# Kernel optimization log

Hardware: AMD Instinct MI355X
Metric: run time of the kernel (lower is better)

## Reference

```python
import jax, jax.numpy as jnp
import numpy as np

B, T, E, S, W, H = 2, 2048, 256, 128, 8, 150

def _mlp(x, w1, b1, w2, b2, w3, b3):
    # Score module: Linear->ReLU->Linear->ReLU->Linear (dropout inactive in eval)
    h = jax.nn.relu(x @ w1 + b1)
    h = jax.nn.relu(h @ w2 + b2)
    return h @ w3 + b3

def _mlp_params(key, d_in):
    k1, k2, k3 = jax.random.split(key, 3)
    s = 0.02
    return (s * jax.random.normal(k1, (d_in, H), jnp.float32), jnp.zeros((H,), jnp.float32),
            s * jax.random.normal(k2, (H, H), jnp.float32), jnp.zeros((H,), jnp.float32),
            s * jax.random.normal(k3, (H, 1), jnp.float32), jnp.zeros((1,), jnp.float32))

def setup_inputs() -> dict:
    key = jax.random.key(0)
    ke, ks, ka, km, kp = jax.random.split(key, 5)
    inp = {
        'batch_embeds': jax.random.normal(ke, (B, T, E), jnp.float32),
        'span_starts': jax.random.randint(ks, (B, S), 0, T - W, jnp.int32),
    }
    for name, k, d in [('attn', ka, E), ('ment', km, 3 * E), ('pair', kp, 9 * E)]:
        w1, b1, w2, b2, w3, b3 = _mlp_params(k, d)
        inp.update({f'{name}_w1': w1, f'{name}_b1': b1, f'{name}_w2': w2,
                    f'{name}_b2': b2, f'{name}_w3': w3, f'{name}_b3': b3})
    return inp

def reference(batch_embeds, span_starts,
              attn_w1, attn_b1, attn_w2, attn_b2, attn_w3, attn_b3,
              ment_w1, ment_b1, ment_w2, ment_b2, ment_w3, ment_b3,
              pair_w1, pair_b1, pair_w2, pair_b2, pair_w3, pair_b3):
    # ---- MentionScore ----
    attns = _mlp(batch_embeds, attn_w1, attn_b1, attn_w2, attn_b2, attn_w3, attn_b3)  # [B,T,1]
    spans = span_starts[:, :, None] + jnp.arange(W)                                   # [B,S,W]
    flat = spans.reshape(B, S * W)
    emb_spans = jnp.take_along_axis(batch_embeds, flat[:, :, None], axis=1).reshape(B, S, W, E)
    attn_spans = jnp.take_along_axis(attns, flat[:, :, None], axis=1).reshape(B, S, W, 1)
    start = emb_spans[:, :, 0, :]
    end = emb_spans[:, :, -1, :]
    weighted = jnp.sum(emb_spans * attn_spans, axis=2)                                # [B,S,E]
    g_i = jnp.concatenate([start, end, weighted], axis=-1)                            # [B,S,3E]
    mention_scores = _mlp(g_i, ment_w1, ment_b1, ment_w2, ment_b2, ment_w3, ment_b3)  # [B,S,1]
    # ---- PairwiseScore: all-pairs cat(g_i, g_j, g_i*g_j) ----
    gi = jnp.broadcast_to(g_i[:, :, None, :], (B, S, S, 3 * E))
    gj = jnp.broadcast_to(g_i[:, None, :, :], (B, S, S, 3 * E))
    pairs = jnp.concatenate([gi, gj, gi * gj], axis=-1)                               # [B,S,S,9E]
    pair_scores = _mlp(pairs, pair_w1, pair_b1, pair_w2, pair_b2, pair_w3, pair_b3)   # [B,S,S,1]
    # extended score = mean(mention_i, mention_j, pair_ij)
    ext = (mention_scores[:, :, None, :] + mention_scores[:, None, :, :] + pair_scores) / 3.0
    return ext
```

## Files before the change

kernel.cpp:

```cpp
#include <hip/hip_runtime.h>
#include <hip/hip_bf16.h>


typedef __bf16 bf16;
typedef __attribute__((ext_vector_type(8))) short v8s;
typedef __attribute__((ext_vector_type(8))) __bf16 v8bf;
typedef __attribute__((ext_vector_type(4))) float v4f;

#define MFMA_BF16(A, B, C) __builtin_amdgcn_mfma_f32_16x16x32_bf16((A), (B), (C), 0, 0, 0)

__device__ __forceinline__ v8bf mul_cvt8(float4 xa, float4 xb, float4 sa, float4 sb) {
    v8bf w;
    w[0] = (bf16)(xa.x * sa.x); w[1] = (bf16)(xa.y * sa.y);
    w[2] = (bf16)(xa.z * sa.z); w[3] = (bf16)(xa.w * sa.w);
    w[4] = (bf16)(xb.x * sb.x); w[5] = (bf16)(xb.y * sb.y);
    w[6] = (bf16)(xb.z * sb.z); w[7] = (bf16)(xb.w * sb.w);
    return w;
}
__device__ __forceinline__ v8bf cvt8(float4 xa, float4 xb) {
    v8bf w;
    w[0] = (bf16)xa.x; w[1] = (bf16)xa.y; w[2] = (bf16)xa.z; w[3] = (bf16)xa.w;
    w[4] = (bf16)xb.x; w[5] = (bf16)xb.y; w[6] = (bf16)xb.z; w[7] = (bf16)xb.w;
    return w;
}

__global__ __launch_bounds__(256) void prep_kernel(
    const float* __restrict__ pw1, const float* __restrict__ pw2,
    const float* __restrict__ aw1, const float* __restrict__ aw2,
    const float* __restrict__ mw1, const float* __restrict__ mw2,
    const float* __restrict__ pb1, const float* __restrict__ pb2, const float* __restrict__ pw3,
    const float* __restrict__ ab1, const float* __restrict__ ab2, const float* __restrict__ aw3,
    const float* __restrict__ mb1, const float* __restrict__ mb2, const float* __restrict__ mw3,
    bf16* __restrict__ w1cT, bf16* __restrict__ w2pT,
    bf16* __restrict__ w1aT, bf16* __restrict__ w2aT, bf16* __restrict__ w2mT,
    bf16* __restrict__ wuvmT, float* __restrict__ bias)
{
    int idx = blockIdx.x * 256 + threadIdx.x;
    if (idx < 147456) {
        int h = idx / 768, e = idx % 768;
        w1cT[idx] = (bf16)((h < 150) ? pw1[(1536 + e) * 150 + h] : 0.f);
    } else if (idx < 178176) {
        int j = idx - 147456; int n = j / 160, k = j % 160;
        w2pT[j] = (bf16)((n < 150 && k < 150) ? pw2[k * 150 + n] : 0.f);
    } else if (idx < 227328) {
        int j = idx - 178176; int h = j / 256, e = j % 256;
        w1aT[j] = (bf16)((h < 150) ? aw1[e * 150 + h] : 0.f);
    } else if (idx < 258048) {
        int j = idx - 227328; int n = j / 160, k = j % 160;
        w2aT[j] = (bf16)((n < 150 && k < 150) ? aw2[k * 150 + n] : 0.f);
    } else if (idx < 288768) {
        int j = idx - 258048; int n = j / 160, k = j % 160;
        w2mT[j] = (bf16)((n < 150 && k < 150) ? mw2[k * 150 + n] : 0.f);
    } else if (idx < 731136) {
        int j = idx - 288768; int s = j / 147456; int r = j % 147456;
        int h = r / 768, e = r % 768;
        float v = 0.f;
        if (h < 150) {
            if (s == 0)      v = pw1[e * 150 + h];
            else if (s == 1) v = pw1[(768 + e) * 150 + h];
            else             v = mw1[e * 150 + h];
        }
        wuvmT[j] = (bf16)v;
    } else if (idx < 732864) {
        int j = idx - 731136; int arr = j / 192, h = j % 192;
        const float* src;
        switch (arr) {
            case 0: src = pb1; break; case 1: src = pb2; break; case 2: src = pw3; break;
            case 3: src = ab1; break; case 4: src = ab2; break; case 5: src = aw3; break;
            case 6: src = mb1; break; case 7: src = mb2; break; default: src = mw3; break;
        }
        bias[j] = (h < 150) ? src[h] : 0.f;
    }
}

__global__ __launch_bounds__(256) void build_g_kernel(
    const float* __restrict__ emb, const int* __restrict__ spans,
    const float* __restrict__ attns, float* __restrict__ g)
{
    int blk = blockIdx.x;
    int b = blk >> 7;
    int t0 = spans[blk];
    int e = threadIdx.x;
    const float* eb = emb + ((size_t)(b * 2048 + t0)) * 256 + e;
    const float* at = attns + b * 2048 + t0;
    float start = eb[0];
    float endv  = eb[7 * 256];
    float wsum = 0.f;
#pragma unroll
    for (int w = 0; w < 8; ++w) wsum = fmaf(eb[w * 256], at[w], wsum);
    g[(size_t)blk * 768 + e]       = start;
    g[(size_t)blk * 768 + 256 + e] = endv;
    g[(size_t)blk * 768 + 512 + e] = wsum;
}

#define A32_ELEMS 2304
#define A64_ELEMS 4608
#define B_ELEMS   13824

__global__ __launch_bounds__(512, 4) void attn_mfma_kernel(
    const float* __restrict__ emb,
    const bf16* __restrict__ w1aT, const bf16* __restrict__ w2aT,
    const float* __restrict__ b1p, const float* __restrict__ b2p,
    const float* __restrict__ w3p, const float* __restrict__ b3,
    float* __restrict__ attns)
{
    __shared__ __attribute__((aligned(16))) char smem[64512];
    bf16*  a_lds  = (bf16*)smem;
    bf16*  b_lds  = (bf16*)(smem + 9216);
    bf16*  h1_lds = (bf16*)smem;
    float* red    = (float*)(smem + 10752);

    const int m0  = blockIdx.x * 32;
    const int tid = threadIdx.x;
    const int lane = tid & 63;
    const int wm = (tid >> 6) >> 2, wn = (tid >> 6) & 3;
    const int l15 = lane & 15, lk = (lane >> 4) * 8;
    const int aj = tid >> 3, ae = (tid & 7) * 8;
    const int br = tid >> 3, bc = (tid & 7) * 8;
    const float* gA = emb + (size_t)(m0 + (aj & 31)) * 256 + ae;

    v4f acc[3];
#pragma unroll
    for (int nf = 0; nf < 3; ++nf) acc[nf] = (v4f){0.f, 0.f, 0.f, 0.f};

#define ATTN_COMPUTE(AB, BB)                                                   \
    do {                                                                       \
        _Pragma("unroll")                                                      \
        for (int ks = 0; ks < 2; ++ks) {                                       \
            const int kb = ks * 32 + lk;                                       \
            v8s af = *(const v8s*)&(AB)[(wm * 16 + l15) * 72 + kb];            \
            v8s bf0 = *(const v8s*)&(BB)[(wn * 48 +  0 + l15) * 72 + kb];      \
            v8s bf1 = *(const v8s*)&(BB)[(wn * 48 + 16 + l15) * 72 + kb];      \
            v8s bf2 = *(const v8s*)&(BB)[(wn * 48 + 32 + l15) * 72 + kb];      \
            acc[0] = MFMA_BF16(af, bf0, acc[0]);                               \
            acc[1] = MFMA_BF16(af, bf1, acc[1]);                               \
            acc[2] = MFMA_BF16(af, bf2, acc[2]);                               \
        }                                                                      \
    } while (0)

    {
        if (tid < 256) {
            float4 x0 = *(const float4*)(gA + 0), x1 = *(const float4*)(gA + 4);
            *(v8bf*)(a_lds + aj * 72 + ae) = cvt8(x0, x1);
        }
#pragma unroll
        for (int s2 = 0; s2 < 3; ++s2) {
            const int row = br + s2 * 64;
            *(uint4*)(b_lds + row * 72 + bc) = *(const uint4*)(w1aT + row * 256 + bc);
        }
    }
    float4 xB0, xB1; uint4 bB0, bB1, bB2;
    if (tid < 256) { xB0 = *(const float4*)(gA + 64); xB1 = *(const float4*)(gA + 68); }
    bB0 = *(const uint4*)(w1aT + (br +   0) * 256 + 64 + bc);
    bB1 = *(const uint4*)(w1aT + (br +  64) * 256 + 64 + bc);
    bB2 = *(const uint4*)(w1aT + (br + 128) * 256 + 64 + bc);
    __syncthreads();

    float4 xA0, xA1; uint4 bA0, bA1, bA2;
    for (int cc = 0; cc < 2; ++cc) {
        const int c = cc * 2;
        if (cc < 1) {
            const int e0 = (c + 2) * 64;
            if (tid < 256) { xA0 = *(const float4*)(gA + e0); xA1 = *(const float4*)(gA + e0 + 4); }
            bA0 = *(const uint4*)(w1aT + (br +   0) * 256 + e0 + bc);
            bA1 = *(const uint4*)(w1aT + (br +  64) * 256 + e0 + bc);
            bA2 = *(const uint4*)(w1aT + (br + 128) * 256 + e0 + bc);
        }
        ATTN_COMPUTE(a_lds, b_lds);
        if (tid < 256)
            *(v8bf*)(a_lds + A32_ELEMS + aj * 72 + ae) = cvt8(xB0, xB1);
        *(uint4*)(b_lds + B_ELEMS + (br +   0) * 72 + bc) = bB0;
        *(uint4*)(b_lds + B_ELEMS + (br +  64) * 72 + bc) = bB1;
        *(uint4*)(b_lds + B_ELEMS + (br + 128) * 72 + bc) = bB2;
        __syncthreads();
        if (cc < 1) {
            const int e0 = (c + 3) * 64;
            if (tid < 256) { xB0 = *(const float4*)(gA + e0); xB1 = *(const float4*)(gA + e0 + 4); }
            bB0 = *(const uint4*)(w1aT + (br +   0) * 256 + e0 + bc);
            bB1 = *(const uint4*)(w1aT + (br +  64) * 256 + e0 + bc);
            bB2 = *(const uint4*)(w1aT + (br + 128) * 256 + e0 + bc);
        }
        ATTN_COMPUTE(a_lds + A32_ELEMS, b_lds + B_ELEMS);
        if (cc < 1) {
            if (tid < 256)
                *(v8bf*)(a_lds + aj * 72 + ae) = cvt8(xA0, xA1);
            *(uint4*)(b_lds + (br +   0) * 72 + bc) = bA0;
            *(uint4*)(b_lds + (br +  64) * 72 + bc) = bA1;
            *(uint4*)(b_lds + (br + 128) * 72 + bc) = bA2;
        }
        __syncthreads();
    }

    {
        const float b10 = b1p[wn * 48 + 0  + l15];
        const float b11 = b1p[wn * 48 + 16 + l15];
        const float b12 = b1p[wn * 48 + 32 + l15];
#pragma unroll
        for (int r = 0; r < 4; ++r) {
            const int jl = wm * 16 + (lane >> 4) * 4 + r;
            bf16* hrow = h1_lds + jl * 168 + wn * 48 + l15;
            hrow[0] = (bf16)fmaxf(acc[0][r] + b10, 0.f);
            if (wn < 3) {
                hrow[16] = (bf16)fmaxf(acc[1][r] + b11, 0.f);
                hrow[32] = (bf16)fmaxf(acc[2][r] + b12, 0.f);
            }
        }
    }
    __syncthreads();

    v4f acc2[3];
#pragma unroll
    for (int nf = 0; nf < 3; ++nf) acc2[nf] = (v4f){0.f, 0.f, 0.f, 0.f};
#pragma unroll
    for (int ks = 0; ks < 5; ++ks) {
        const int kb = ks * 32 + lk;
        v8s af = *(const v8s*)&h1_lds[(wm * 16 + l15) * 168 + kb];
        v8s bfr[3];
#pragma unroll
        for (int nf = 0; nf < 3; ++nf)
            bfr[nf] = *(const v8s*)&w2aT[(size_t)(wn * 48 + nf * 16 + l15) * 160 + kb];
#pragma unroll
        for (int nf = 0; nf < 3; ++nf)
            acc2[nf] = MFMA_BF16(af, bfr[nf], acc2[nf]);
    }

    const float b2v0 = b2p[wn * 48 + 0  + l15], w3v0 = w3p[wn * 48 + 0  + l15];
    const float b2v1 = b2p[wn * 48 + 16 + l15], w3v1 = w3p[wn * 48 + 16 + l15];
    const float b2v2 = b2p[wn * 48 + 32 + l15], w3v2 = w3p[wn * 48 + 32 + l15];
#pragma unroll
    for (int r = 0; r < 4; ++r) {
        float p = fmaxf(acc2[0][r] + b2v0, 0.f) * w3v0
                + fmaxf(acc2[1][r] + b2v1, 0.f) * w3v1
                + fmaxf(acc2[2][r] + b2v2, 0.f) * w3v2;
        p += __shfl_xor(p, 1);
        p += __shfl_xor(p, 2);
        p += __shfl_xor(p, 4);
        p += __shfl_xor(p, 8);
        if (l15 == 0) {
            const int jl = wm * 16 + (lane >> 4) * 4 + r;
            red[jl * 4 + wn] = p;
        }
    }
    __syncthreads();
    if (tid < 32) {
        attns[m0 + tid] = red[tid * 4 + 0] + red[tid * 4 + 1]
                        + red[tid * 4 + 2] + red[tid * 4 + 3] + b3[0];
    }
}

__global__ __launch_bounds__(512, 4) void uvm_mfma_kernel(
    const float* __restrict__ g, const bf16* __restrict__ wuvmT,
    const bf16* __restrict__ w2mT,
    const float* __restrict__ pb1p, const float* __restrict__ mb1p,
    const float* __restrict__ mb2p, const float* __restrict__ mw3p,
    const float* __restrict__ mb3,
    float* __restrict__ u_pad, float* __restrict__ v_pad, float* __restrict__ ment)
{
    __shared__ __attribute__((aligned(16))) char smem[64512];
    bf16*  a_lds  = (bf16*)smem;
    bf16*  b_lds  = (bf16*)(smem + 9216);
    bf16*  h1_lds = (bf16*)smem;
    float* red    = (float*)(smem + 10752);

    const int sect = blockIdx.x >> 3;
    const int m0   = (blockIdx.x & 7) * 32;
    const bf16* Bw = wuvmT + (size_t)sect * 147456;
    const int tid = threadIdx.x;
    const int lane = tid & 63;
    const int wm = (tid >> 6) >> 2, wn = (tid >> 6) & 3;
    const int l15 = lane & 15, lk = (lane >> 4) * 8;
    const int aj = tid >> 3, ae = (tid & 7) * 8;
    const int br = tid >> 3, bc = (tid & 7) * 8;
    const float* gA = g + (size_t)(m0 + (aj & 31)) * 768 + ae;

    v4f acc[3];
#pragma unroll
    for (int nf = 0; nf < 3; ++nf) acc[nf] = (v4f){0.f, 0.f, 0.f, 0.f};

    {
        if (tid < 256) {
            float4 x0 = *(const float4*)(gA + 0), x1 = *(const float4*)(gA + 4);
            *(v8bf*)(a_lds + aj * 72 + ae) = cvt8(x0, x1);
        }
#pragma unroll
        for (int s2 = 0; s2 < 3; ++s2) {
            const int row = br + s2 * 64;
            *(uint4*)(b_lds + row * 72 + bc) = *(const uint4*)(Bw + row * 768 + bc);
        }
    }
    float4 xB0, xB1; uint4 bB0, bB1, bB2;
    if (tid < 256) { xB0 = *(const float4*)(gA + 64); xB1 = *(const float4*)(gA + 68); }
    bB0 = *(const uint4*)(Bw + (br +   0) * 768 + 64 + bc);
    bB1 = *(const uint4*)(Bw + (br +  64) * 768 + 64 + bc);
    bB2 = *(const uint4*)(Bw + (br + 128) * 768 + 64 + bc);
    __syncthreads();

    float4 xA0, xA1; uint4 bA0, bA1, bA2;
    for (int cc = 0; cc < 6; ++cc) {
        const int c = cc * 2;
        if (cc < 5) {
            const int e0 = (c + 2) * 64;
            if (tid < 256) { xA0 = *(const float4*)(gA + e0); xA1 = *(const float4*)(gA + e0 + 4); }
            bA0 = *(const uint4*)(Bw + (br +   0) * 768 + e0 + bc);
            bA1 = *(const uint4*)(Bw + (br +  64) * 768 + e0 + bc);
            bA2 = *(const uint4*)(Bw + (br + 128) * 768 + e0 + bc);
        }
        ATTN_COMPUTE(a_lds, b_lds);
        if (tid < 256)
            *(v8bf*)(a_lds + A32_ELEMS + aj * 72 + ae) = cvt8(xB0, xB1);
        *(uint4*)(b_lds + B_ELEMS + (br +   0) * 72 + bc) = bB0;
        *(uint4*)(b_lds + B_ELEMS + (br +  64) * 72 + bc) = bB1;
        *(uint4*)(b_lds + B_ELEMS + (br + 128) * 72 + bc) = bB2;
        __syncthreads();
        if (cc < 5) {
            const int e0 = (c + 3) * 64;
            if (tid < 256) { xB0 = *(const float4*)(gA + e0); xB1 = *(const float4*)(gA + e0 + 4); }
            bB0 = *(const uint4*)(Bw + (br +   0) * 768 + e0 + bc);
            bB1 = *(const uint4*)(Bw + (br +  64) * 768 + e0 + bc);
            bB2 = *(const uint4*)(Bw + (br + 128) * 768 + e0 + bc);
        }
        ATTN_COMPUTE(a_lds + A32_ELEMS, b_lds + B_ELEMS);
        if (cc < 5) {
            if (tid < 256)
                *(v8bf*)(a_lds + aj * 72 + ae) = cvt8(xA0, xA1);
            *(uint4*)(b_lds + (br +   0) * 72 + bc) = bA0;
            *(uint4*)(b_lds + (br +  64) * 72 + bc) = bA1;
            *(uint4*)(b_lds + (br + 128) * 72 + bc) = bA2;
        }
        __syncthreads();
    }

    if (sect < 2) {
        float* dst = (sect == 0) ? u_pad : v_pad;
        const float bb0 = (sect == 0) ? pb1p[wn * 48 + 0  + l15] : 0.f;
        const float bb1 = (sect == 0) ? pb1p[wn * 48 + 16 + l15] : 0.f;
        const float bb2 = (sect == 0) ? pb1p[wn * 48 + 32 + l15] : 0.f;
#pragma unroll
        for (int r = 0; r < 4; ++r) {
            const int jl = wm * 16 + (lane >> 4) * 4 + r;
            float* drow = dst + (size_t)(m0 + jl) * 192 + wn * 48 + l15;
            drow[0]  = acc[0][r] + bb0;
            drow[16] = acc[1][r] + bb1;
            drow[32] = acc[2][r] + bb2;
        }
        return;
    }

    {
        const float b10 = mb1p[wn * 48 + 0  + l15];
        const float b11 = mb1p[wn * 48 + 16 + l15];
        const float b12 = mb1p[wn * 48 + 32 + l15];
#pragma unroll
        for (int r = 0; r < 4; ++r) {
            const int jl = wm * 16 + (lane >> 4) * 4 + r;
            bf16* hrow = h1_lds + jl * 168 + wn * 48 + l15;
            hrow[0] = (bf16)fmaxf(acc[0][r] + b10, 0.f);
            if (wn < 3) {
                hrow[16] = (bf16)fmaxf(acc[1][r] + b11, 0.f);
                hrow[32] = (bf16)fmaxf(acc[2][r] + b12, 0.f);
            }
        }
    }
    __syncthreads();

    v4f acc2[3];
#pragma unroll
    for (int nf = 0; nf < 3; ++nf) acc2[nf] = (v4f){0.f, 0.f, 0.f, 0.f};
#pragma unroll
    for (int ks = 0; ks < 5; ++ks) {
        const int kb = ks * 32 + lk;
        v8s af = *(const v8s*)&h1_lds[(wm * 16 + l15) * 168 + kb];
        v8s bfr[3];
#pragma unroll
        for (int nf = 0; nf < 3; ++nf)
            bfr[nf] = *(const v8s*)&w2mT[(size_t)(wn * 48 + nf * 16 + l15) * 160 + kb];
#pragma unroll
        for (int nf = 0; nf < 3; ++nf)
            acc2[nf] = MFMA_BF16(af, bfr[nf], acc2[nf]);
    }

    const float b2v0 = mb2p[wn * 48 + 0  + l15], w3v0 = mw3p[wn * 48 + 0  + l15];
    const float b2v1 = mb2p[wn * 48 + 16 + l15], w3v1 = mw3p[wn * 48 + 16 + l15];
    const float b2v2 = mb2p[wn * 48 + 32 + l15], w3v2 = mw3p[wn * 48 + 32 + l15];
#pragma unroll
    for (int r = 0; r < 4; ++r) {
        float p = fmaxf(acc2[0][r] + b2v0, 0.f) * w3v0
                + fmaxf(acc2[1][r] + b2v1, 0.f) * w3v1
                + fmaxf(acc2[2][r] + b2v2, 0.f) * w3v2;
        p += __shfl_xor(p, 1);
        p += __shfl_xor(p, 2);
        p += __shfl_xor(p, 4);
        p += __shfl_xor(p, 8);
        if (l15 == 0) {
            const int jl = wm * 16 + (lane >> 4) * 4 + r;
            red[jl * 4 + wn] = p;
        }
    }
    __syncthreads();
    if (tid < 32) {
        ment[m0 + tid] = red[tid * 4 + 0] + red[tid * 4 + 1]
                       + red[tid * 4 + 2] + red[tid * 4 + 3] + mb3[0];
    }
}

__global__ __launch_bounds__(512, 4) void pair_mfma_kernel(
    const float* __restrict__ g,
    const float* __restrict__ u_pad, const float* __restrict__ v_pad,
    const bf16* __restrict__ w1cT, const bf16* __restrict__ w2T,
    const float* __restrict__ b2_pad, const float* __restrict__ w3_pad,
    const float* __restrict__ pb3, const float* __restrict__ ment,
    float* __restrict__ out)
{
    __shared__ __attribute__((aligned(16))) char smem[76800];
    bf16*  a_lds  = (bf16*)smem;
    bf16*  b_lds  = (bf16*)(smem + 18432);
    float* gi_s   = (float*)(smem + 73728);
    bf16*  h1_lds = (bf16*)smem;
    float* red    = (float*)(smem + 22528);

    const int blk = blockIdx.x;
    const int b = blk >> 8;
    const int i = (blk >> 1) & 127;
    const int half = blk & 1;
    const int row_i = b * 128 + i;
    const int jg0 = b * 128 + half * 64;
    const int tid = threadIdx.x;
    const int lane = tid & 63;
    const int wm = (tid >> 6) >> 2, wn = (tid >> 6) & 3;
    const int l15 = lane & 15, lk = (lane >> 4) * 8;
    const int aj = tid >> 3, ae = (tid & 7) * 8;
    const int br = tid >> 3, bc = (tid & 7) * 8;
    const float* gA = g + (size_t)(jg0 + aj) * 768 + ae;

    if (tid < 192)
        *(float4*)&gi_s[tid * 4] = *(const float4*)&g[(size_t)row_i * 768 + tid * 4];
    __syncthreads();

    v4f acc[2][3];
#pragma unroll
    for (int mf = 0; mf < 2; ++mf)
#pragma unroll
        for (int nf = 0; nf < 3; ++nf) acc[mf][nf] = (v4f){0.f, 0.f, 0.f, 0.f};

#define PAIR_COMPUTE(AB, BB)                                                   \
    do {                                                                       \
        _Pragma("unroll")                                                      \
        for (int ks = 0; ks < 2; ++ks) {                                       \
            const int kb = ks * 32 + lk;                                       \
            v8s af0 = *(const v8s*)&(AB)[(wm * 32 +  0 + l15) * 72 + kb];      \
            v8s af1 = *(const v8s*)&(AB)[(wm * 32 + 16 + l15) * 72 + kb];      \
            v8s bf0 = *(const v8s*)&(BB)[(wn * 48 +  0 + l15) * 72 + kb];      \
            v8s bf1 = *(const v8s*)&(BB)[(wn * 48 + 16 + l15) * 72 + kb];      \
            v8s bf2 = *(const v8s*)&(BB)[(wn * 48 + 32 + l15) * 72 + kb];      \
            acc[0][0] = MFMA_BF16(af0, bf0, acc[0][0]);                        \
            acc[0][1] = MFMA_BF16(af0, bf1, acc[0][1]);                        \
            acc[0][2] = MFMA_BF16(af0, bf2, acc[0][2]);                        \
            acc[1][0] = MFMA_BF16(af1, bf0, acc[1][0]);                        \
            acc[1][1] = MFMA_BF16(af1, bf1, acc[1][1]);                        \
            acc[1][2] = MFMA_BF16(af1, bf2, acc[1][2]);                        \
        }                                                                      \
    } while (0)

    {
        float4 x0 = *(const float4*)(gA + 0), x1 = *(const float4*)(gA + 4);
        const float* gp = gi_s + ae;
        float4 s0 = *(const float4*)(gp + 0), s1 = *(const float4*)(gp + 4);
        *(v8bf*)(a_lds + aj * 72 + ae) = mul_cvt8(x0, x1, s0, s1);
#pragma unroll
        for (int s2 = 0; s2 < 3; ++s2) {
            const int row = br + s2 * 64;
            *(uint4*)(b_lds + row * 72 + bc) = *(const uint4*)(w1cT + row * 768 + bc);
        }
    }
    float4 xB0, xB1; uint4 bB0, bB1, bB2;
    xB0 = *(const float4*)(gA + 64);
    xB1 = *(const float4*)(gA + 68);
    bB0 = *(const uint4*)(w1cT + (br +   0) * 768 + 64 + bc);
    bB1 = *(const uint4*)(w1cT + (br +  64) * 768 + 64 + bc);
    bB2 = *(const uint4*)(w1cT + (br + 128) * 768 + 64 + bc);
    __syncthreads();

    float4 xA0, xA1; uint4 bA0, bA1, bA2;
    for (int cc = 0; cc < 6; ++cc) {
        const int c = cc * 2;
        if (cc < 5) {
            const int e0 = (c + 2) * 64;
            xA0 = *(const float4*)(gA + e0);
            xA1 = *(const float4*)(gA + e0 + 4);
            bA0 = *(const uint4*)(w1cT + (br +   0) * 768 + e0 + bc);
            bA1 = *(const uint4*)(w1cT + (br +  64) * 768 + e0 + bc);
            bA2 = *(const uint4*)(w1cT + (br + 128) * 768 + e0 + bc);
        }
        PAIR_COMPUTE(a_lds, b_lds);
        {
            const float* gp = gi_s + (c + 1) * 64 + ae;
            float4 s0 = *(const float4*)(gp + 0), s1 = *(const float4*)(gp + 4);
            *(v8bf*)(a_lds + A64_ELEMS + aj * 72 + ae) = mul_cvt8(xB0, xB1, s0, s1);
            *(uint4*)(b_lds + B_ELEMS + (br +   0) * 72 + bc) = bB0;
            *(uint4*)(b_lds + B_ELEMS + (br +  64) * 72 + bc) = bB1;
            *(uint4*)(b_lds + B_ELEMS + (br + 128) * 72 + bc) = bB2;
        }
        __syncthreads();
        if (cc < 5) {
            const int e0 = (c + 3) * 64;
            xB0 = *(const float4*)(gA + e0);
            xB1 = *(const float4*)(gA + e0 + 4);
            bB0 = *(const uint4*)(w1cT + (br +   0) * 768 + e0 + bc);
            bB1 = *(const uint4*)(w1cT + (br +  64) * 768 + e0 + bc);
            bB2 = *(const uint4*)(w1cT + (br + 128) * 768 + e0 + bc);
        }
        PAIR_COMPUTE(a_lds + A64_ELEMS, b_lds + B_ELEMS);
        if (cc < 5) {
            const float* gp = gi_s + (c + 2) * 64 + ae;
            float4 s0 = *(const float4*)(gp + 0), s1 = *(const float4*)(gp + 4);
            *(v8bf*)(a_lds + aj * 72 + ae) = mul_cvt8(xA0, xA1, s0, s1);
            *(uint4*)(b_lds + (br +   0) * 72 + bc) = bA0;
            *(uint4*)(b_lds + (br +  64) * 72 + bc) = bA1;
            *(uint4*)(b_lds + (br + 128) * 72 + bc) = bA2;
        }
        __syncthreads();
    }

    {
        const float uh0 = u_pad[row_i * 192 + wn * 48 + 0  + l15];
        const float uh1 = u_pad[row_i * 192 + wn * 48 + 16 + l15];
        const float uh2 = u_pad[row_i * 192 + wn * 48 + 32 + l15];
#pragma unroll
        for (int mf = 0; mf < 2; ++mf) {
#pragma unroll
            for (int r = 0; r < 4; ++r) {
                const int jl = wm * 32 + mf * 16 + (lane >> 4) * 4 + r;
                const float* vrow = v_pad + (size_t)(jg0 + jl) * 192 + wn * 48 + l15;
                const float v0 = acc[mf][0][r] + uh0 + vrow[0];
                const float v1 = acc[mf][1][r] + uh1 + vrow[16];
                const float v2 = acc[mf][2][r] + uh2 + vrow[32];
                bf16* hrow = h1_lds + jl * 168 + wn * 48 + l15;
                hrow[0] = (bf16)fmaxf(v0, 0.f);
                if (wn < 3) {
                    hrow[16] = (bf16)fmaxf(v1, 0.f);
                    hrow[32] = (bf16)fmaxf(v2, 0.f);
                }
            }
        }
    }
    __syncthreads();

    v4f acc2[2][3];
#pragma unroll
    for (int mf = 0; mf < 2; ++mf)
#pragma unroll
        for (int nf = 0; nf < 3; ++nf) acc2[mf][nf] = (v4f){0.f, 0.f, 0.f, 0.f};
#pragma unroll
    for (int ks = 0; ks < 5; ++ks) {
        const int kb = ks * 32 + lk;
        v8s af[2], bfr[3];
#pragma unroll
        for (int mf = 0; mf < 2; ++mf)
            af[mf] = *(const v8s*)&h1_lds[(wm * 32 + mf * 16 + l15) * 168 + kb];
#pragma unroll
        for (int nf = 0; nf < 3; ++nf)
            bfr[nf] = *(const v8s*)&w2T[(size_t)(wn * 48 + nf * 16 + l15) * 160 + kb];
#pragma unroll
        for (int mf = 0; mf < 2; ++mf)
#pragma unroll
            for (int nf = 0; nf < 3; ++nf)
                acc2[mf][nf] = MFMA_BF16(af[mf], bfr[nf], acc2[mf][nf]);
    }

    const float b2v0 = b2_pad[wn * 48 + 0  + l15], w3v0 = w3_pad[wn * 48 + 0  + l15];
    const float b2v1 = b2_pad[wn * 48 + 16 + l15], w3v1 = w3_pad[wn * 48 + 16 + l15];
    const float b2v2 = b2_pad[wn * 48 + 32 + l15], w3v2 = w3_pad[wn * 48 + 32 + l15];
#pragma unroll
    for (int mf = 0; mf < 2; ++mf) {
#pragma unroll
        for (int r = 0; r < 4; ++r) {
            float p = fmaxf(acc2[mf][0][r] + b2v0, 0.f) * w3v0
                    + fmaxf(acc2[mf][1][r] + b2v1, 0.f) * w3v1
                    + fmaxf(acc2[mf][2][r] + b2v2, 0.f) * w3v2;
            p += __shfl_xor(p, 1);
            p += __shfl_xor(p, 2);
            p += __shfl_xor(p, 4);
            p += __shfl_xor(p, 8);
            if (l15 == 0) {
                const int jl = wm * 32 + mf * 16 + (lane >> 4) * 4 + r;
                red[jl * 4 + wn] = p;
            }
        }
    }
    __syncthreads();
    if (tid < 64) {
        const float s = red[tid * 4 + 0] + red[tid * 4 + 1] + red[tid * 4 + 2] + red[tid * 4 + 3];
        out[(size_t)b * 16384 + (size_t)i * 128 + half * 64 + tid] =
            (s + pb3[0] + ment[row_i] + ment[b * 128 + half * 64 + tid]) * (1.f / 3.f);
    }
}

extern "C" void kernel_launch(void* const* d_in, const int* in_sizes, int n_in,
                              void* d_out, int out_size, void* d_ws, size_t ws_size,
                              hipStream_t stream)
{
    const float* emb   = (const float*)d_in[0];
    const int*   spans = (const int*)d_in[1];
    const float* aw1 = (const float*)d_in[2];
    const float* ab1 = (const float*)d_in[3];
    const float* aw2 = (const float*)d_in[4];
    const float* ab2 = (const float*)d_in[5];
    const float* aw3 = (const float*)d_in[6];
    const float* ab3 = (const float*)d_in[7];
    const float* mw1 = (const float*)d_in[8];
    const float* mb1 = (const float*)d_in[9];
    const float* mw2 = (const float*)d_in[10];
    const float* mb2 = (const float*)d_in[11];
    const float* mw3 = (const float*)d_in[12];
    const float* mb3 = (const float*)d_in[13];
    const float* pw1 = (const float*)d_in[14];
    const float* pb1 = (const float*)d_in[15];
    const float* pw2 = (const float*)d_in[16];
    const float* pb2 = (const float*)d_in[17];
    const float* pw3 = (const float*)d_in[18];
    const float* pb3 = (const float*)d_in[19];

    float* ws    = (float*)d_ws;
    float* attns = ws;
    float* g     = ws + 4096;
    float* ment  = ws + 200704;
    float* u_pad = ws + 200960;
    float* v_pad = ws + 250112;
    float* bias  = ws + 299264;
    float* pb1p = bias;         float* pb2p = bias + 192;  float* pw3p = bias + 384;
    float* ab1p = bias + 576;   float* ab2p = bias + 768;  float* aw3p = bias + 960;
    float* mb1p = bias + 1152;  float* mb2p = bias + 1344; float* mw3p = bias + 1536;
    bf16* w1cT  = (bf16*)(ws + 300992);
    bf16* w2pT  = (bf16*)(ws + 374720);
    bf16* w1aT  = (bf16*)(ws + 390080);
    bf16* w2aT  = (bf16*)(ws + 414656);
    bf16* w2mT  = (bf16*)(ws + 430016);
    bf16* wuvmT = (bf16*)(ws + 445376);

    prep_kernel<<<2863, 256, 0, stream>>>(pw1, pw2, aw1, aw2, mw1, mw2,
                                          pb1, pb2, pw3, ab1, ab2, aw3, mb1, mb2, mw3,
                                          w1cT, w2pT, w1aT, w2aT, w2mT, wuvmT, bias);
    attn_mfma_kernel<<<128, 512, 0, stream>>>(emb, w1aT, w2aT, ab1p, ab2p, aw3p, ab3, attns);
    build_g_kernel<<<256, 256, 0, stream>>>(emb, spans, attns, g);
    uvm_mfma_kernel<<<24, 512, 0, stream>>>(g, wuvmT, w2mT, pb1p, mb1p, mb2p, mw3p, mb3,
                                            u_pad, v_pad, ment);
    pair_mfma_kernel<<<512, 512, 0, stream>>>(g, u_pad, v_pad, w1cT, w2pT,
                                              pb2p, pw3p, pb3, ment, (float*)d_out);
}
```

Measured before the change: 57.67 us.

## Widen pair tile to 128 rows and load W1 fragments straight to registers

The pair kernel now handles all 128 j-rows for one i per block, which halves the grid to 256 blocks and doubles the M tile per wave (4 MFMA row fragments). The W1 fragments are no longer staged in LDS. Each wave loads its B operands directly from global memory into registers and prefetches the next chunk. This removes the LDS traffic for the weight tile, halves redundant weight loads across blocks, and shrinks shared memory. The trade-off is higher register pressure (launch bounds drop to 2 blocks per SM) and fewer blocks, which gives less parallelism on a GPU with many CUs.

```diff
diff --git a/kernel.cpp b/kernel.cpp
--- a/kernel.cpp
+++ b/kernel.cpp
@@ -94,7 +94,6 @@
 }
 
 #define A32_ELEMS 2304
-#define A64_ELEMS 4608
 #define B_ELEMS   13824
 
 __global__ __launch_bounds__(512, 4) void attn_mfma_kernel(
@@ -403,7 +402,8 @@
     }
 }
 
-__global__ __launch_bounds__(512, 4) void pair_mfma_kernel(
+#define A128_ELEMS 9216
+__global__ __launch_bounds__(512, 2) void pair_mfma_kernel(
     const float* __restrict__ g,
     const float* __restrict__ u_pad, const float* __restrict__ v_pad,
     const bf16* __restrict__ w1cT, const bf16* __restrict__ w2T,
@@ -411,112 +411,92 @@
     const float* __restrict__ pb3, const float* __restrict__ ment,
     float* __restrict__ out)
 {
-    __shared__ __attribute__((aligned(16))) char smem[76800];
+    __shared__ __attribute__((aligned(16))) char smem[45056];
     bf16*  a_lds  = (bf16*)smem;
-    bf16*  b_lds  = (bf16*)(smem + 18432);
-    float* gi_s   = (float*)(smem + 73728);
+    float* gi_s   = (float*)(smem + 36864);
     bf16*  h1_lds = (bf16*)smem;
-    float* red    = (float*)(smem + 22528);
+    float* red    = (float*)(smem + 43008);
 
     const int blk = blockIdx.x;
-    const int b = blk >> 8;
-    const int i = (blk >> 1) & 127;
-    const int half = blk & 1;
-    const int row_i = b * 128 + i;
-    const int jg0 = b * 128 + half * 64;
+    const int b = blk >> 7;
+    const int i = blk & 127;
+    const int row_i = blk;
+    const int jg0 = b * 128;
     const int tid = threadIdx.x;
     const int lane = tid & 63;
     const int wm = (tid >> 6) >> 2, wn = (tid >> 6) & 3;
     const int l15 = lane & 15, lk = (lane >> 4) * 8;
-    const int aj = tid >> 3, ae = (tid & 7) * 8;
-    const int br = tid >> 3, bc = (tid & 7) * 8;
+    const int aj = tid >> 2, ae = (tid & 3) * 16;
     const float* gA = g + (size_t)(jg0 + aj) * 768 + ae;
+    const bf16*  bP = w1cT + (size_t)(wn * 48 + l15) * 768 + lk;
 
     if (tid < 192)
         *(float4*)&gi_s[tid * 4] = *(const float4*)&g[(size_t)row_i * 768 + tid * 4];
     __syncthreads();
 
-    v4f acc[2][3];
-#pragma unroll
-    for (int mf = 0; mf < 2; ++mf)
+    {
+        float4 x0 = *(const float4*)(gA + 0),  x1 = *(const float4*)(gA + 4);
+        float4 x2 = *(const float4*)(gA + 8),  x3 = *(const float4*)(gA + 12);
+        const float* gp = gi_s + ae;
+        float4 s0 = *(const float4*)(gp + 0),  s1 = *(const float4*)(gp + 4);
+        float4 s2 = *(const float4*)(gp + 8),  s3 = *(const float4*)(gp + 12);
+        bf16* ad = a_lds + aj * 72 + ae;
+        *(v8bf*)ad       = mul_cvt8(x0, x1, s0, s1);
+        *(v8bf*)(ad + 8) = mul_cvt8(x2, x3, s2, s3);
+    }
+    v8s cb[2][3];
+#pragma unroll
+    for (int ks = 0; ks < 2; ++ks)
+#pragma unroll
+        for (int nf = 0; nf < 3; ++nf)
+            cb[ks][nf] = *(const v8s*)(bP + nf * 12288 + ks * 32);
+    __syncthreads();
+
+    v4f acc[4][3];
+#pragma unroll
+    for (int mf = 0; mf < 4; ++mf)
 #pragma unroll
         for (int nf = 0; nf < 3; ++nf) acc[mf][nf] = (v4f){0.f, 0.f, 0.f, 0.f};
 
-#define PAIR_COMPUTE(AB, BB)                                                   \
-    do {                                                                       \
-        _Pragma("unroll")                                                      \
-        for (int ks = 0; ks < 2; ++ks) {                                       \
-            const int kb = ks * 32 + lk;                                       \
-            v8s af0 = *(const v8s*)&(AB)[(wm * 32 +  0 + l15) * 72 + kb];      \
-            v8s af1 = *(const v8s*)&(AB)[(wm * 32 + 16 + l15) * 72 + kb];      \
-            v8s bf0 = *(const v8s*)&(BB)[(wn * 48 +  0 + l15) * 72 + kb];      \
-            v8s bf1 = *(const v8s*)&(BB)[(wn * 48 + 16 + l15) * 72 + kb];      \
-            v8s bf2 = *(const v8s*)&(BB)[(wn * 48 + 32 + l15) * 72 + kb];      \
-            acc[0][0] = MFMA_BF16(af0, bf0, acc[0][0]);                        \
-            acc[0][1] = MFMA_BF16(af0, bf1, acc[0][1]);                        \
-            acc[0][2] = MFMA_BF16(af0, bf2, acc[0][2]);                        \
-            acc[1][0] = MFMA_BF16(af1, bf0, acc[1][0]);                        \
-            acc[1][1] = MFMA_BF16(af1, bf1, acc[1][1]);                        \
-            acc[1][2] = MFMA_BF16(af1, bf2, acc[1][2]);                        \
-        }                                                                      \
-    } while (0)
-
-    {
-        float4 x0 = *(const float4*)(gA + 0), x1 = *(const float4*)(gA + 4);
-        const float* gp = gi_s + ae;
-        float4 s0 = *(const float4*)(gp + 0), s1 = *(const float4*)(gp + 4);
-        *(v8bf*)(a_lds + aj * 72 + ae) = mul_cvt8(x0, x1, s0, s1);
-#pragma unroll
-        for (int s2 = 0; s2 < 3; ++s2) {
-            const int row = br + s2 * 64;
-            *(uint4*)(b_lds + row * 72 + bc) = *(const uint4*)(w1cT + row * 768 + bc);
-        }
-    }
-    float4 xB0, xB1; uint4 bB0, bB1, bB2;
-    xB0 = *(const float4*)(gA + 64);
-    xB1 = *(const float4*)(gA + 68);
-    bB0 = *(const uint4*)(w1cT + (br +   0) * 768 + 64 + bc);
-    bB1 = *(const uint4*)(w1cT + (br +  64) * 768 + 64 + bc);
-    bB2 = *(const uint4*)(w1cT + (br + 128) * 768 + 64 + bc);
-    __syncthreads();
-
-    float4 xA0, xA1; uint4 bA0, bA1, bA2;
-    for (int cc = 0; cc < 6; ++cc) {
-        const int c = cc * 2;
-        if (cc < 5) {
-            const int e0 = (c + 2) * 64;
-            xA0 = *(const float4*)(gA + e0);
-            xA1 = *(const float4*)(gA + e0 + 4);
-            bA0 = *(const uint4*)(w1cT + (br +   0) * 768 + e0 + bc);
-            bA1 = *(const uint4*)(w1cT + (br +  64) * 768 + e0 + bc);
-            bA2 = *(const uint4*)(w1cT + (br + 128) * 768 + e0 + bc);
-        }
-        PAIR_COMPUTE(a_lds, b_lds);
-        {
+    for (int c = 0; c < 12; ++c) {
+        float4 xn0, xn1, xn2, xn3;
+        v8s pb[2][3];
+        if (c < 11) {
+            const int e0 = (c + 1) * 64;
+            xn0 = *(const float4*)(gA + e0);      xn1 = *(const float4*)(gA + e0 + 4);
+            xn2 = *(const float4*)(gA + e0 + 8);  xn3 = *(const float4*)(gA + e0 + 12);
+#pragma unroll
+            for (int ks = 0; ks < 2; ++ks)
+#pragma unroll
+                for (int nf = 0; nf < 3; ++nf)
+                    pb[ks][nf] = *(const v8s*)(bP + nf * 12288 + e0 + ks * 32);
+        }
+        const bf16* ab = a_lds + (c & 1) * A128_ELEMS;
+#pragma unroll
+        for (int ks = 0; ks < 2; ++ks) {
+            const int kb = ks * 32 + lk;
+            v8s af[4];
+#pragma unroll
+            for (int mf = 0; mf < 4; ++mf)
+                af[mf] = *(const v8s*)&ab[(wm * 64 + mf * 16 + l15) * 72 + kb];
+#pragma unroll
+            for (int mf = 0; mf < 4; ++mf)
+#pragma unroll
+                for (int nf = 0; nf < 3; ++nf)
+                    acc[mf][nf] = MFMA_BF16(af[mf], cb[ks][nf], acc[mf][nf]);
+        }
+        if (c < 11) {
             const float* gp = gi_s + (c + 1) * 64 + ae;
-            float4 s0 = *(const float4*)(gp + 0), s1 = *(const float4*)(gp + 4);
-            *(v8bf*)(a_lds + A64_ELEMS + aj * 72 + ae) = mul_cvt8(xB0, xB1, s0, s1);
-            *(uint4*)(b_lds + B_ELEMS + (br +   0) * 72 + bc) = bB0;
-            *(uint4*)(b_lds + B_ELEMS + (br +  64) * 72 + bc) = bB1;
-            *(uint4*)(b_lds + B_ELEMS + (br + 128) * 72 + bc) = bB2;
-        }
-        __syncthreads();
-        if (cc < 5) {
-            const int e0 = (c + 3) * 64;
-            xB0 = *(const float4*)(gA + e0);
-            xB1 = *(const float4*)(gA + e0 + 4);
-            bB0 = *(const uint4*)(w1cT + (br +   0) * 768 + e0 + bc);
-            bB1 = *(const uint4*)(w1cT + (br +  64) * 768 + e0 + bc);
-            bB2 = *(const uint4*)(w1cT + (br + 128) * 768 + e0 + bc);
-        }
-        PAIR_COMPUTE(a_lds + A64_ELEMS, b_lds + B_ELEMS);
-        if (cc < 5) {
-            const float* gp = gi_s + (c + 2) * 64 + ae;
-            float4 s0 = *(const float4*)(gp + 0), s1 = *(const float4*)(gp + 4);
-            *(v8bf*)(a_lds + aj * 72 + ae) = mul_cvt8(xA0, xA1, s0, s1);
-            *(uint4*)(b_lds + (br +   0) * 72 + bc) = bA0;
-            *(uint4*)(b_lds + (br +  64) * 72 + bc) = bA1;
-            *(uint4*)(b_lds + (br + 128) * 72 + bc) = bA2;
+            float4 s0 = *(const float4*)(gp + 0),  s1 = *(const float4*)(gp + 4);
+            float4 s2 = *(const float4*)(gp + 8),  s3 = *(const float4*)(gp + 12);
+            bf16* ad = a_lds + ((c + 1) & 1) * A128_ELEMS + aj * 72 + ae;
+            *(v8bf*)ad       = mul_cvt8(xn0, xn1, s0, s1);
+            *(v8bf*)(ad + 8) = mul_cvt8(xn2, xn3, s2, s3);
+#pragma unroll
+            for (int ks = 0; ks < 2; ++ks)
+#pragma unroll
+                for (int nf = 0; nf < 3; ++nf)
+                    cb[ks][nf] = pb[ks][nf];
         }
         __syncthreads();
     }
@@ -526,10 +506,10 @@
         const float uh1 = u_pad[row_i * 192 + wn * 48 + 16 + l15];
         const float uh2 = u_pad[row_i * 192 + wn * 48 + 32 + l15];
 #pragma unroll
-        for (int mf = 0; mf < 2; ++mf) {
+        for (int mf = 0; mf < 4; ++mf) {
 #pragma unroll
             for (int r = 0; r < 4; ++r) {
-                const int jl = wm * 32 + mf * 16 + (lane >> 4) * 4 + r;
+                const int jl = wm * 64 + mf * 16 + (lane >> 4) * 4 + r;
                 const float* vrow = v_pad + (size_t)(jg0 + jl) * 192 + wn * 48 + l15;
                 const float v0 = acc[mf][0][r] + uh0 + vrow[0];
                 const float v1 = acc[mf][1][r] + uh1 + vrow[16];
@@ -545,23 +525,23 @@
     }
     __syncthreads();
 
-    v4f acc2[2][3];
-#pragma unroll
-    for (int mf = 0; mf < 2; ++mf)
+    v4f acc2[4][3];
+#pragma unroll
+    for (int mf = 0; mf < 4; ++mf)
 #pragma unroll
         for (int nf = 0; nf < 3; ++nf) acc2[mf][nf] = (v4f){0.f, 0.f, 0.f, 0.f};
 #pragma unroll
     for (int ks = 0; ks < 5; ++ks) {
         const int kb = ks * 32 + lk;
-        v8s af[2], bfr[3];
-#pragma unroll
-        for (int mf = 0; mf < 2; ++mf)
-            af[mf] = *(const v8s*)&h1_lds[(wm * 32 + mf * 16 + l15) * 168 + kb];
+        v8s af[4], bfr[3];
+#pragma unroll
+        for (int mf = 0; mf < 4; ++mf)
+            af[mf] = *(const v8s*)&h1_lds[(wm * 64 + mf * 16 + l15) * 168 + kb];
 #pragma unroll
         for (int nf = 0; nf < 3; ++nf)
             bfr[nf] = *(const v8s*)&w2T[(size_t)(wn * 48 + nf * 16 + l15) * 160 + kb];
 #pragma unroll
-        for (int mf = 0; mf < 2; ++mf)
+        for (int mf = 0; mf < 4; ++mf)
 #pragma unroll
             for (int nf = 0; nf < 3; ++nf)
                 acc2[mf][nf] = MFMA_BF16(af[mf], bfr[nf], acc2[mf][nf]);
@@ -571,7 +551,7 @@
     const float b2v1 = b2_pad[wn * 48 + 16 + l15], w3v1 = w3_pad[wn * 48 + 16 + l15];
     const float b2v2 = b2_pad[wn * 48 + 32 + l15], w3v2 = w3_pad[wn * 48 + 32 + l15];
 #pragma unroll
-    for (int mf = 0; mf < 2; ++mf) {
+    for (int mf = 0; mf < 4; ++mf) {
 #pragma unroll
         for (int r = 0; r < 4; ++r) {
             float p = fmaxf(acc2[mf][0][r] + b2v0, 0.f) * w3v0
@@ -582,16 +562,16 @@
             p += __shfl_xor(p, 4);
             p += __shfl_xor(p, 8);
             if (l15 == 0) {
-                const int jl = wm * 32 + mf * 16 + (lane >> 4) * 4 + r;
+                const int jl = wm * 64 + mf * 16 + (lane >> 4) * 4 + r;
                 red[jl * 4 + wn] = p;
             }
         }
     }
     __syncthreads();
-    if (tid < 64) {
+    if (tid < 128) {
         const float s = red[tid * 4 + 0] + red[tid * 4 + 1] + red[tid * 4 + 2] + red[tid * 4 + 3];
-        out[(size_t)b * 16384 + (size_t)i * 128 + half * 64 + tid] =
-            (s + pb3[0] + ment[row_i] + ment[b * 128 + half * 64 + tid]) * (1.f / 3.f);
+        out[(size_t)blk * 128 + tid] =
+            (s + pb3[0] + ment[row_i] + ment[jg0 + tid]) * (1.f / 3.f);
     }
 }
 
@@ -644,6 +624,6 @@
     build_g_kernel<<<256, 256, 0, stream>>>(emb, spans, attns, g);
     uvm_mfma_kernel<<<24, 512, 0, stream>>>(g, wuvmT, w2mT, pb1p, mb1p, mb2p, mw3p, mb3,
                                             u_pad, v_pad, ment);
-    pair_mfma_kernel<<<512, 512, 0, stream>>>(g, u_pad, v_pad, w1cT, w2pT,
+    pair_mfma_kernel<<<256, 512, 0, stream>>>(g, u_pad, v_pad, w1cT, w2pT,
                                               pb2p, pw3p, pb3, ment, (float*)d_out);
 }
```

Result: slower. 74.00 us (+28.3%).

## Process full 128-row j tile per block in pair kernel to halve weight reloads

Applied to the files above, without the earlier changes.

Each pair-kernel block now handles all 128 j rows for one i instead of 64, doubling the per-warp M tile (4 MFMA row fragments). The W1 slices in w1cT are streamed from global into LDS once per i rather than twice, and the grid is halved to 256 blocks. In exchange, LDS use and register pressure rise (launch bounds lowered to 2 blocks per SM), and with only 256 blocks some compute units may sit idle, reducing parallelism.

```diff
diff --git a/kernel.cpp b/kernel.cpp
--- a/kernel.cpp
+++ b/kernel.cpp
@@ -94,7 +94,6 @@
 }
 
 #define A32_ELEMS 2304
-#define A64_ELEMS 4608
 #define B_ELEMS   13824
 
 __global__ __launch_bounds__(512, 4) void attn_mfma_kernel(
@@ -403,7 +402,8 @@
     }
 }
 
-__global__ __launch_bounds__(512, 4) void pair_mfma_kernel(
+#define A128_ELEMS 9216
+__global__ __launch_bounds__(512, 2) void pair_mfma_kernel(
     const float* __restrict__ g,
     const float* __restrict__ u_pad, const float* __restrict__ v_pad,
     const bf16* __restrict__ w1cT, const bf16* __restrict__ w2T,
@@ -411,24 +411,22 @@
     const float* __restrict__ pb3, const float* __restrict__ ment,
     float* __restrict__ out)
 {
-    __shared__ __attribute__((aligned(16))) char smem[76800];
+    __shared__ __attribute__((aligned(16))) char smem[95232];
     bf16*  a_lds  = (bf16*)smem;
-    bf16*  b_lds  = (bf16*)(smem + 18432);
-    float* gi_s   = (float*)(smem + 73728);
+    bf16*  b_lds  = (bf16*)(smem + 36864);
+    float* gi_s   = (float*)(smem + 92160);
     bf16*  h1_lds = (bf16*)smem;
-    float* red    = (float*)(smem + 22528);
+    float* red    = (float*)(smem + 43008);
 
     const int blk = blockIdx.x;
-    const int b = blk >> 8;
-    const int i = (blk >> 1) & 127;
-    const int half = blk & 1;
-    const int row_i = b * 128 + i;
-    const int jg0 = b * 128 + half * 64;
+    const int b = blk >> 7;
+    const int row_i = blk;
+    const int jg0 = b * 128;
     const int tid = threadIdx.x;
     const int lane = tid & 63;
     const int wm = (tid >> 6) >> 2, wn = (tid >> 6) & 3;
     const int l15 = lane & 15, lk = (lane >> 4) * 8;
-    const int aj = tid >> 3, ae = (tid & 7) * 8;
+    const int aj = tid >> 2, ae = (tid & 3) * 16;
     const int br = tid >> 3, bc = (tid & 7) * 8;
     const float* gA = g + (size_t)(jg0 + aj) * 768 + ae;
 
@@ -436,9 +434,9 @@
         *(float4*)&gi_s[tid * 4] = *(const float4*)&g[(size_t)row_i * 768 + tid * 4];
     __syncthreads();
 
-    v4f acc[2][3];
-#pragma unroll
-    for (int mf = 0; mf < 2; ++mf)
+    v4f acc[4][3];
+#pragma unroll
+    for (int mf = 0; mf < 4; ++mf)
 #pragma unroll
         for (int nf = 0; nf < 3; ++nf) acc[mf][nf] = (v4f){0.f, 0.f, 0.f, 0.f};
 
@@ -447,8 +445,10 @@
         _Pragma("unroll")                                                      \
         for (int ks = 0; ks < 2; ++ks) {                                       \
             const int kb = ks * 32 + lk;                                       \
-            v8s af0 = *(const v8s*)&(AB)[(wm * 32 +  0 + l15) * 72 + kb];      \
-            v8s af1 = *(const v8s*)&(AB)[(wm * 32 + 16 + l15) * 72 + kb];      \
+            v8s af0 = *(const v8s*)&(AB)[(wm * 64 +  0 + l15) * 72 + kb];      \
+            v8s af1 = *(const v8s*)&(AB)[(wm * 64 + 16 + l15) * 72 + kb];      \
+            v8s af2 = *(const v8s*)&(AB)[(wm * 64 + 32 + l15) * 72 + kb];      \
+            v8s af3 = *(const v8s*)&(AB)[(wm * 64 + 48 + l15) * 72 + kb];      \
             v8s bf0 = *(const v8s*)&(BB)[(wn * 48 +  0 + l15) * 72 + kb];      \
             v8s bf1 = *(const v8s*)&(BB)[(wn * 48 + 16 + l15) * 72 + kb];      \
             v8s bf2 = *(const v8s*)&(BB)[(wn * 48 + 32 + l15) * 72 + kb];      \
@@ -458,35 +458,45 @@
             acc[1][0] = MFMA_BF16(af1, bf0, acc[1][0]);                        \
             acc[1][1] = MFMA_BF16(af1, bf1, acc[1][1]);                        \
             acc[1][2] = MFMA_BF16(af1, bf2, acc[1][2]);                        \
+            acc[2][0] = MFMA_BF16(af2, bf0, acc[2][0]);                        \
+            acc[2][1] = MFMA_BF16(af2, bf1, acc[2][1]);                        \
+            acc[2][2] = MFMA_BF16(af2, bf2, acc[2][2]);                        \
+            acc[3][0] = MFMA_BF16(af3, bf0, acc[3][0]);                        \
+            acc[3][1] = MFMA_BF16(af3, bf1, acc[3][1]);                        \
+            acc[3][2] = MFMA_BF16(af3, bf2, acc[3][2]);                        \
         }                                                                      \
     } while (0)
 
     {
-        float4 x0 = *(const float4*)(gA + 0), x1 = *(const float4*)(gA + 4);
+        float4 x0 = *(const float4*)(gA + 0),  x1 = *(const float4*)(gA + 4);
+        float4 x2 = *(const float4*)(gA + 8),  x3 = *(const float4*)(gA + 12);
         const float* gp = gi_s + ae;
-        float4 s0 = *(const float4*)(gp + 0), s1 = *(const float4*)(gp + 4);
-        *(v8bf*)(a_lds + aj * 72 + ae) = mul_cvt8(x0, x1, s0, s1);
-#pragma unroll
-        for (int s2 = 0; s2 < 3; ++s2) {
-            const int row = br + s2 * 64;
+        float4 s0 = *(const float4*)(gp + 0),  s1 = *(const float4*)(gp + 4);
+        float4 s2 = *(const float4*)(gp + 8),  s3 = *(const float4*)(gp + 12);
+        bf16* ad = a_lds + aj * 72 + ae;
+        *(v8bf*)ad       = mul_cvt8(x0, x1, s0, s1);
+        *(v8bf*)(ad + 8) = mul_cvt8(x2, x3, s2, s3);
+#pragma unroll
+        for (int s2i = 0; s2i < 3; ++s2i) {
+            const int row = br + s2i * 64;
             *(uint4*)(b_lds + row * 72 + bc) = *(const uint4*)(w1cT + row * 768 + bc);
         }
     }
-    float4 xB0, xB1; uint4 bB0, bB1, bB2;
-    xB0 = *(const float4*)(gA + 64);
-    xB1 = *(const float4*)(gA + 68);
+    float4 xB0, xB1, xB2, xB3; uint4 bB0, bB1, bB2;
+    xB0 = *(const float4*)(gA + 64); xB1 = *(const float4*)(gA + 68);
+    xB2 = *(const float4*)(gA + 72); xB3 = *(const float4*)(gA + 76);
     bB0 = *(const uint4*)(w1cT + (br +   0) * 768 + 64 + bc);
     bB1 = *(const uint4*)(w1cT + (br +  64) * 768 + 64 + bc);
     bB2 = *(const uint4*)(w1cT + (br + 128) * 768 + 64 + bc);
     __syncthreads();
 
-    float4 xA0, xA1; uint4 bA0, bA1, bA2;
+    float4 xA0, xA1, xA2, xA3; uint4 bA0, bA1, bA2;
     for (int cc = 0; cc < 6; ++cc) {
         const int c = cc * 2;
         if (cc < 5) {
             const int e0 = (c + 2) * 64;
-            xA0 = *(const float4*)(gA + e0);
-            xA1 = *(const float4*)(gA + e0 + 4);
+            xA0 = *(const float4*)(gA + e0);      xA1 = *(const float4*)(gA + e0 + 4);
+            xA2 = *(const float4*)(gA + e0 + 8);  xA3 = *(const float4*)(gA + e0 + 12);
             bA0 = *(const uint4*)(w1cT + (br +   0) * 768 + e0 + bc);
             bA1 = *(const uint4*)(w1cT + (br +  64) * 768 + e0 + bc);
             bA2 = *(const uint4*)(w1cT + (br + 128) * 768 + e0 + bc);
@@ -494,8 +504,11 @@
         PAIR_COMPUTE(a_lds, b_lds);
         {
             const float* gp = gi_s + (c + 1) * 64 + ae;
-            float4 s0 = *(const float4*)(gp + 0), s1 = *(const float4*)(gp + 4);
-            *(v8bf*)(a_lds + A64_ELEMS + aj * 72 + ae) = mul_cvt8(xB0, xB1, s0, s1);
+            float4 s0 = *(const float4*)(gp + 0),  s1 = *(const float4*)(gp + 4);
+            float4 s2 = *(const float4*)(gp + 8),  s3 = *(const float4*)(gp + 12);
+            bf16* ad = a_lds + A128_ELEMS + aj * 72 + ae;
+            *(v8bf*)ad       = mul_cvt8(xB0, xB1, s0, s1);
+            *(v8bf*)(ad + 8) = mul_cvt8(xB2, xB3, s2, s3);
             *(uint4*)(b_lds + B_ELEMS + (br +   0) * 72 + bc) = bB0;
             *(uint4*)(b_lds + B_ELEMS + (br +  64) * 72 + bc) = bB1;
             *(uint4*)(b_lds + B_ELEMS + (br + 128) * 72 + bc) = bB2;
@@ -503,17 +516,20 @@
         __syncthreads();
         if (cc < 5) {
             const int e0 = (c + 3) * 64;
-            xB0 = *(const float4*)(gA + e0);
-            xB1 = *(const float4*)(gA + e0 + 4);
+            xB0 = *(const float4*)(gA + e0);      xB1 = *(const float4*)(gA + e0 + 4);
+            xB2 = *(const float4*)(gA + e0 + 8);  xB3 = *(const float4*)(gA + e0 + 12);
             bB0 = *(const uint4*)(w1cT + (br +   0) * 768 + e0 + bc);
             bB1 = *(const uint4*)(w1cT + (br +  64) * 768 + e0 + bc);
             bB2 = *(const uint4*)(w1cT + (br + 128) * 768 + e0 + bc);
         }
-        PAIR_COMPUTE(a_lds + A64_ELEMS, b_lds + B_ELEMS);
+        PAIR_COMPUTE(a_lds + A128_ELEMS, b_lds + B_ELEMS);
         if (cc < 5) {
             const float* gp = gi_s + (c + 2) * 64 + ae;
-            float4 s0 = *(const float4*)(gp + 0), s1 = *(const float4*)(gp + 4);
-            *(v8bf*)(a_lds + aj * 72 + ae) = mul_cvt8(xA0, xA1, s0, s1);
+            float4 s0 = *(const float4*)(gp + 0),  s1 = *(const float4*)(gp + 4);
+            float4 s2 = *(const float4*)(gp + 8),  s3 = *(const float4*)(gp + 12);
+            bf16* ad = a_lds + aj * 72 + ae;
+            *(v8bf*)ad       = mul_cvt8(xA0, xA1, s0, s1);
+            *(v8bf*)(ad + 8) = mul_cvt8(xA2, xA3, s2, s3);
             *(uint4*)(b_lds + (br +   0) * 72 + bc) = bA0;
             *(uint4*)(b_lds + (br +  64) * 72 + bc) = bA1;
             *(uint4*)(b_lds + (br + 128) * 72 + bc) = bA2;
@@ -526,10 +542,10 @@
         const float uh1 = u_pad[row_i * 192 + wn * 48 + 16 + l15];
         const float uh2 = u_pad[row_i * 192 + wn * 48 + 32 + l15];
 #pragma unroll
-        for (int mf = 0; mf < 2; ++mf) {
+        for (int mf = 0; mf < 4; ++mf) {
 #pragma unroll
             for (int r = 0; r < 4; ++r) {
-                const int jl = wm * 32 + mf * 16 + (lane >> 4) * 4 + r;
+                const int jl = wm * 64 + mf * 16 + (lane >> 4) * 4 + r;
                 const float* vrow = v_pad + (size_t)(jg0 + jl) * 192 + wn * 48 + l15;
                 const float v0 = acc[mf][0][r] + uh0 + vrow[0];
                 const float v1 = acc[mf][1][r] + uh1 + vrow[16];
@@ -545,23 +561,23 @@
     }
     __syncthreads();
 
-    v4f acc2[2][3];
-#pragma unroll
-    for (int mf = 0; mf < 2; ++mf)
+    v4f acc2[4][3];
+#pragma unroll
+    for (int mf = 0; mf < 4; ++mf)
 #pragma unroll
         for (int nf = 0; nf < 3; ++nf) acc2[mf][nf] = (v4f){0.f, 0.f, 0.f, 0.f};
 #pragma unroll
     for (int ks = 0; ks < 5; ++ks) {
         const int kb = ks * 32 + lk;
-        v8s af[2], bfr[3];
-#pragma unroll
-        for (int mf = 0; mf < 2; ++mf)
-            af[mf] = *(const v8s*)&h1_lds[(wm * 32 + mf * 16 + l15) * 168 + kb];
+        v8s af[4], bfr[3];
+#pragma unroll
+        for (int mf = 0; mf < 4; ++mf)
+            af[mf] = *(const v8s*)&h1_lds[(wm * 64 + mf * 16 + l15) * 168 + kb];
 #pragma unroll
         for (int nf = 0; nf < 3; ++nf)
             bfr[nf] = *(const v8s*)&w2T[(size_t)(wn * 48 + nf * 16 + l15) * 160 + kb];
 #pragma unroll
-        for (int mf = 0; mf < 2; ++mf)
+        for (int mf = 0; mf < 4; ++mf)
 #pragma unroll
             for (int nf = 0; nf < 3; ++nf)
                 acc2[mf][nf] = MFMA_BF16(af[mf], bfr[nf], acc2[mf][nf]);
@@ -571,7 +587,7 @@
     const float b2v1 = b2_pad[wn * 48 + 16 + l15], w3v1 = w3_pad[wn * 48 + 16 + l15];
     const float b2v2 = b2_pad[wn * 48 + 32 + l15], w3v2 = w3_pad[wn * 48 + 32 + l15];
 #pragma unroll
-    for (int mf = 0; mf < 2; ++mf) {
+    for (int mf = 0; mf < 4; ++mf) {
 #pragma unroll
         for (int r = 0; r < 4; ++r) {
             float p = fmaxf(acc2[mf][0][r] + b2v0, 0.f) * w3v0
@@ -582,16 +598,16 @@
             p += __shfl_xor(p, 4);
             p += __shfl_xor(p, 8);
             if (l15 == 0) {
-                const int jl = wm * 32 + mf * 16 + (lane >> 4) * 4 + r;
+                const int jl = wm * 64 + mf * 16 + (lane >> 4) * 4 + r;
                 red[jl * 4 + wn] = p;
             }
         }
     }
     __syncthreads();
-    if (tid < 64) {
+    if (tid < 128) {
         const float s = red[tid * 4 + 0] + red[tid * 4 + 1] + red[tid * 4 + 2] + red[tid * 4 + 3];
-        out[(size_t)b * 16384 + (size_t)i * 128 + half * 64 + tid] =
-            (s + pb3[0] + ment[row_i] + ment[b * 128 + half * 64 + tid]) * (1.f / 3.f);
+        out[(size_t)blk * 128 + tid] =
+            (s + pb3[0] + ment[row_i] + ment[jg0 + tid]) * (1.f / 3.f);
     }
 }
 
@@ -644,6 +660,6 @@
     build_g_kernel<<<256, 256, 0, stream>>>(emb, spans, attns, g);
     uvm_mfma_kernel<<<24, 512, 0, stream>>>(g, wuvmT, w2mT, pb1p, mb1p, mb2p, mw3p, mb3,
                                             u_pad, v_pad, ment);
-    pair_mfma_kernel<<<512, 512, 0, stream>>>(g, u_pad, v_pad, w1cT, w2pT,
+    pair_mfma_kernel<<<256, 512, 0, stream>>>(g, u_pad, v_pad, w1cT, w2pT,
                                               pb2p, pw3p, pb3, ment, (float*)d_out);
 }
```

After: 62.70 us. 8.7% more time.
